# Kernel tuning notes

Measured on AMD Instinct MI355X. Metric: run time of the kernel, lower is better.

## Reference

```python
import jax, jax.numpy as jnp
import numpy as np

E = 8        # n_routed_experts
K = 4        # num_experts_per_tok
T = 1024     # tokens
H = 1024     # hidden_size
I = 1408     # moe_intermediate_size


def setup_inputs() -> dict:
    key = jax.random.key(0)
    ks = jax.random.split(key, 6)
    hidden_states = jax.random.normal(ks[0], (T, H), jnp.float32)
    rw = jax.random.uniform(ks[1], (T, K), jnp.float32)
    router_weights = rw / jnp.sum(rw, axis=-1, keepdims=True)  # normalized top-k router weights
    selected_experts = jax.random.randint(ks[2], (T, K), 0, E, jnp.int32)
    gate_w = jax.random.normal(ks[3], (E, H, I), jnp.float32) * (H ** -0.5)  # lecun_normal-ish
    up_w = jax.random.normal(ks[4], (E, H, I), jnp.float32) * (H ** -0.5)
    down_w = jax.random.normal(ks[5], (E, I, H), jnp.float32) * (I ** -0.5)
    return {
        'hidden_states': hidden_states,
        'router_weights': router_weights,
        'gate_w': gate_w,
        'up_w': up_w,
        'down_w': down_w,
        'selected_experts': selected_experts,
    }


def _grouped_matmul(x, w, seg):
    # x: [m, k] tokens sorted by expert; w: [E, k, n]; seg: [m] expert id per row.
    # Grouped GEMM expressed as E masked GEMMs (fixed small loop over experts);
    # a custom kernel would do true variable-group-size grouped GEMM.
    out = jnp.zeros((x.shape[0], w.shape[-1]), x.dtype)
    for e in range(w.shape[0]):
        out = out + jnp.where((seg == e)[:, None], x, jnp.zeros((), x.dtype)) @ w[e]
    return out


def reference(hidden_states, router_weights, gate_w, up_w, down_w, selected_experts):
    t, k = selected_experts.shape
    flat = selected_experts.ravel()                       # [t*k]
    hs = jnp.repeat(hidden_states, k, axis=0)             # [t*k, H]
    sort_idx = jnp.argsort(flat)                          # dispatch: sort tokens by expert
    seg = flat[sort_idx]
    xs = hs[sort_idx]
    gate = _grouped_matmul(xs, gate_w, seg)               # [t*k, I]
    up = _grouped_matmul(xs, up_w, seg)                   # [t*k, I]
    h = jax.nn.silu(gate) * up                            # fused SwiGLU
    down = _grouped_matmul(h, down_w, seg)                # [t*k, H]
    unsort = jnp.argsort(sort_idx)                        # scatter back to token order
    out = down[unsort].reshape(t, k, -1)
    return jnp.sum(out * router_weights[..., None], axis=1)  # weighted combine [t, H]
```

## Files before the change

### kernel.cpp

```cpp
#include <hip/hip_runtime.h>
#include <hip/hip_bf16.h>
#include <cstdint>
#include <cstddef>

#define NE 8
#define NT 1024
#define NK 4
#define NH 1024
#define NI 1408
#define NA (NT * NK)
#define BM 128
#define MAXTILES 40
#define PADSLOTS 5120

typedef short short8 __attribute__((ext_vector_type(8)));
typedef float f32x4 __attribute__((ext_vector_type(4)));
typedef float f4v __attribute__((ext_vector_type(4)));
typedef unsigned short u16;

#define WS_HDR   0
#define WS_SORT  1024
#define WS_XBF   21504
#define WS_GT    2118656
#define WS_UT    25187328
#define WS_DT    48256000
#define WS_HB    71324672
#define WS_SLOT  (WS_HB + 4992 * NI * 2)

__device__ __forceinline__ u16 f2b(float f) {
  union { float f; uint32_t u; } c; c.f = f;
  uint32_t u = c.u;
  return (u16)((u + 0x7FFFu + ((u >> 16) & 1u)) >> 16);
}

__device__ __forceinline__ void llds16(const void* g, void* l) {
  __builtin_amdgcn_global_load_lds(
      (const __attribute__((address_space(1))) void*)g,
      (__attribute__((address_space(3))) void*)l, 16, 0, 0);
}

__device__ __forceinline__ void transcvt_stripe(const float* __restrict__ src,
                                                u16* __restrict__ dst,
                                                int K, int N, int k0, int n0,
                                                u16* smem, int tid) {
  u16 (*t2)[64][64] = (u16(*)[64][64])smem;
  int r = tid >> 4, c = tid & 15;
  f4v v[2][4];
#pragma unroll
  for (int t = 0; t < 2; ++t)
#pragma unroll
    for (int i = 0; i < 4; ++i)
      v[t][i] = __builtin_nontemporal_load(
          (const f4v*)&src[(size_t)(k0 + r + 16 * i) * N + n0 + t * 64 + c * 4]);
#pragma unroll
  for (int t = 0; t < 2; ++t)
#pragma unroll
    for (int i = 0; i < 4; ++i) {
      ushort4 o;
      o.x = f2b(v[t][i].x); o.y = f2b(v[t][i].y); o.z = f2b(v[t][i].z); o.w = f2b(v[t][i].w);
      int row = r + 16 * i;
      int sc = (c * 4) ^ (row & 56);
      *(ushort4*)&t2[t][row][sc] = o;
    }
  __syncthreads();
#pragma unroll
  for (int t = 0; t < 2; ++t)
#pragma unroll
    for (int i = 0; i < 2; ++i) {
      int idx = i * 256 + tid;
      int n = idx >> 3, kc = idx & 7;
      int cs = n ^ (kc * 8);
      u16 o[8];
#pragma unroll
      for (int j = 0; j < 8; ++j) o[j] = t2[t][kc * 8 + j][cs];
      *(short8*)&dst[(size_t)(n0 + t * 64 + n) * K + k0 + kc * 8] = *(const short8*)o;
    }
}

__global__ __launch_bounds__(256) void k1_prep(
    const float* __restrict__ gw, const float* __restrict__ uw, const float* __restrict__ dw,
    const float* __restrict__ hs, const int* __restrict__ sel,
    u16* __restrict__ gT, u16* __restrict__ uT, u16* __restrict__ dT, u16* __restrict__ xbf,
    int* __restrict__ hdr, int* __restrict__ sorted, int* __restrict__ slotOf) {
  int tid = threadIdx.x;
  int y = blockIdx.y;
  if (y == 24) {
    for (int i = blockIdx.x * 256 + tid; i * 4 < NT * NH; i += 176 * 256) {
      f4v v = __builtin_nontemporal_load((const f4v*)&hs[i * 4]);
      ushort4 o;
      o.x = f2b(v.x); o.y = f2b(v.y); o.z = f2b(v.z); o.w = f2b(v.w);
      *(ushort4*)&xbf[i * 4] = o;
    }
    return;
  }
  if (y == 25) {
    if (blockIdx.x != 0) return;
    __shared__ int cnt[NE], fill[NE], poff_s[NE + 1];
    if (tid < NE) { cnt[tid] = 0; fill[tid] = 0; }
    __syncthreads();
    for (int i = tid; i < NA; i += 256) atomicAdd(&cnt[sel[i]], 1);
    __syncthreads();
    if (tid == 0) {
      int off = 0, nt = 0;
      for (int e = 0; e < NE; ++e) {
        poff_s[e] = off;
        int tiles = (cnt[e] + BM - 1) / BM;
        for (int j = 0; j < tiles; ++j) { hdr[32 + nt] = e; hdr[80 + nt] = off + j * BM; ++nt; }
        off += tiles * BM;
      }
      poff_s[NE] = off;
      hdr[17] = nt;
      for (int e = 0; e < NE; ++e) hdr[e] = cnt[e];
      for (int e = 0; e <= NE; ++e) hdr[8 + e] = poff_s[e];
    }
    __syncthreads();
    for (int i = tid; i < PADSLOTS; i += 256) sorted[i] = -1;
    __syncthreads();
    for (int i = tid; i < NA; i += 256) {
      int e = sel[i];
      int p = atomicAdd(&fill[e], 1);
      int s = poff_s[e] + p;
      sorted[s] = i;
      slotOf[i] = s;
    }
    return;
  }
  __shared__ u16 smem[2 * 64 * 64];
  if (y < 16) {
    int tensor = y >> 3, e = y & 7;
    const float* src = ((tensor == 0) ? gw : uw) + (size_t)e * NH * NI;
    u16* dst = ((tensor == 0) ? gT : uT) + (size_t)e * NH * NI;
    int nb = blockIdx.x % 11, kb = blockIdx.x / 11;
    transcvt_stripe(src, dst, NH, NI, kb * 64, nb * 128, smem, tid);
  } else {
    int e = y - 16;
    const float* src = dw + (size_t)e * NI * NH;
    u16* dst = dT + (size_t)e * NI * NH;
    int nb = blockIdx.x % 8, kb = blockIdx.x / 8;
    transcvt_stripe(src, dst, NI, NH, kb * 64, nb * 128, smem, tid);
  }
}

__global__ __launch_bounds__(256, 2) void k2_gemm1(
    const u16* __restrict__ xbf, const u16* __restrict__ gT, const u16* __restrict__ uT,
    u16* __restrict__ hbuf, const int* __restrict__ hdr, const int* __restrict__ sorted) {
  __shared__ u16 smem[36864];
  int b = blockIdx.x;
  int tid = threadIdx.x;

  int job = (b & 7) * 55 + (b >> 3);
  int tile = job % 40;
  if (tile >= hdr[17]) return;
  int e = hdr[32 + tile];
  int slot0 = hdr[80 + tile];
  int n0 = (job / 40) * 128;

  const u16* aptr[2];
  const u16 *bgp[2], *bup[2];
#pragma unroll
  for (int s = 0; s < 2; ++s) {
    int idx = s * 256 + tid;
    int row = idx >> 2, c = idx & 3;
    int kc = c ^ (row & 3) ^ ((row >> 2) & 3);
    int as = sorted[slot0 + row];
    int trow = (as >= 0) ? (as >> 2) : 0;
    aptr[s] = xbf + (size_t)trow * NH + kc * 8;
    size_t o = ((size_t)e * NI + n0 + row) * NH + kc * 8;
    bgp[s] = gT + o; bup[s] = uT + o;
  }

  int lane = tid & 63, wave = tid >> 6;
  int wm = wave >> 1, wn = wave & 1;
  int l15 = lane & 15, quad = lane >> 4;
  int pos = ((quad ^ (l15 & 3) ^ ((l15 >> 2) & 3)) & 3) * 8;

  f32x4 accg[4][4] = {}; f32x4 accu[4][4] = {};

#define K2_STAGE(BUF, KT)                                                \
  {                                                                      \
    int ko_ = (KT) * 32;                                                 \
    u16* p_ = smem + (BUF) * 12288;                                      \
    llds16(aptr[0] + ko_, p_ + tid * 8);                                 \
    llds16(aptr[1] + ko_, p_ + (256 + tid) * 8);                         \
    llds16(bgp[0] + ko_, p_ + 4096 + tid * 8);                           \
    llds16(bgp[1] + ko_, p_ + 4096 + (256 + tid) * 8);                   \
    llds16(bup[0] + ko_, p_ + 8192 + tid * 8);                           \
    llds16(bup[1] + ko_, p_ + 8192 + (256 + tid) * 8);                   \
  }

  K2_STAGE(0, 0);
  K2_STAGE(1, 1);
  for (int kt = 0; kt < 32; ++kt) {
    if (kt == 31) { asm volatile("s_waitcnt vmcnt(0)" ::: "memory"); }
    else          { asm volatile("s_waitcnt vmcnt(6)" ::: "memory"); }
    __builtin_amdgcn_s_barrier();
    __builtin_amdgcn_sched_barrier(0);
    if (kt < 30) K2_STAGE((kt + 2) % 3, kt + 2);
    const u16* sA  = smem + (kt % 3) * 12288;
    const u16* sBg = sA + 4096;
    const u16* sBu = sA + 8192;
    short8 av[4], bg[4], bu[4];
#pragma unroll
    for (int mf = 0; mf < 4; ++mf)
      av[mf] = *(const short8*)&sA[(wm * 64 + mf * 16 + l15) * 32 + pos];
#pragma unroll
    for (int nf = 0; nf < 4; ++nf) {
      bg[nf] = *(const short8*)&sBg[(wn * 64 + nf * 16 + l15) * 32 + pos];
      bu[nf] = *(const short8*)&sBu[(wn * 64 + nf * 16 + l15) * 32 + pos];
    }
#pragma unroll
    for (int mf = 0; mf < 4; ++mf)
#pragma unroll
      for (int nf = 0; nf < 4; ++nf) {
        accg[mf][nf] = __builtin_amdgcn_mfma_f32_16x16x32_bf16(av[mf], bg[nf], accg[mf][nf], 0, 0, 0);
        accu[mf][nf] = __builtin_amdgcn_mfma_f32_16x16x32_bf16(av[mf], bu[nf], accu[mf][nf], 0, 0, 0);
      }
  }
#undef K2_STAGE

  for (int mf = 0; mf < 4; ++mf)
    for (int nf = 0; nf < 4; ++nf)
      for (int r = 0; r < 4; ++r) {
        int row = wm * 64 + mf * 16 + quad * 4 + r;
        int col = n0 + wn * 64 + nf * 16 + l15;
        float g2 = accg[mf][nf][r], u = accu[mf][nf][r];
        float hv = (g2 / (1.f + __expf(-g2))) * u;
        hbuf[(size_t)(slot0 + row) * NI + col] = f2b(hv);
      }
}

__global__ __launch_bounds__(256, 3) void k3_gemm2(
    const u16* __restrict__ hbuf, const u16* __restrict__ dT,
    const float* __restrict__ rw, float* __restrict__ part,
    const int* __restrict__ hdr, const int* __restrict__ sorted) {
  __shared__ u16 smem[24576];
  int b = blockIdx.x;
  int tile = b >> 3;
  if (tile >= hdr[17]) return;
  int e = hdr[32 + tile];
  int slot0 = hdr[80 + tile];
  int n0 = (b & 7) * 128;
  int tid = threadIdx.x;

  const u16 *ap[2], *bp[2];
#pragma unroll
  for (int s = 0; s < 2; ++s) {
    int idx = s * 256 + tid;
    int row = idx >> 2, c = idx & 3;
    int kc = c ^ (row & 3) ^ ((row >> 2) & 3);
    ap[s] = hbuf + (size_t)(slot0 + row) * NI + kc * 8;
    bp[s] = dT + ((size_t)e * NH + n0 + row) * NI + kc * 8;
  }

  int lane = tid & 63, wave = tid >> 6;
  int wm = wave >> 1, wn = wave & 1;
  int l15 = lane & 15, quad = lane >> 4;
  int pos = ((quad ^ (l15 & 3) ^ ((l15 >> 2) & 3)) & 3) * 8;

  f32x4 acc[4][4] = {};

#define K3_STAGE(BUF, KT)                                                \
  {                                                                      \
    int ko_ = (KT) * 32;                                                 \
    u16* p_ = smem + (BUF) * 8192;                                       \
    llds16(ap[0] + ko_, p_ + tid * 8);                                   \
    llds16(ap[1] + ko_, p_ + (256 + tid) * 8);                           \
    llds16(bp[0] + ko_, p_ + 4096 + tid * 8);                            \
    llds16(bp[1] + ko_, p_ + 4096 + (256 + tid) * 8);                    \
  }

  K3_STAGE(0, 0);
  K3_STAGE(1, 1);
  for (int kt = 0; kt < 44; ++kt) {
    if (kt == 43) { asm volatile("s_waitcnt vmcnt(0)" ::: "memory"); }
    else          { asm volatile("s_waitcnt vmcnt(4)" ::: "memory"); }
    __builtin_amdgcn_s_barrier();
    __builtin_amdgcn_sched_barrier(0);
    if (kt < 42) K3_STAGE((kt + 2) % 3, kt + 2);
    const u16* sA = smem + (kt % 3) * 8192;
    const u16* sB = sA + 4096;
    short8 av[4], bv[4];
#pragma unroll
    for (int mf = 0; mf < 4; ++mf)
      av[mf] = *(const short8*)&sA[(wm * 64 + mf * 16 + l15) * 32 + pos];
#pragma unroll
    for (int nf = 0; nf < 4; ++nf)
      bv[nf] = *(const short8*)&sB[(wn * 64 + nf * 16 + l15) * 32 + pos];
#pragma unroll
    for (int mf = 0; mf < 4; ++mf)
#pragma unroll
      for (int nf = 0; nf < 4; ++nf)
        acc[mf][nf] = __builtin_amdgcn_mfma_f32_16x16x32_bf16(av[mf], bv[nf], acc[mf][nf], 0, 0, 0);
  }
#undef K3_STAGE

  for (int mf = 0; mf < 4; ++mf) {
    int rowb = wm * 64 + mf * 16 + quad * 4;
    for (int r = 0; r < 4; ++r) {
      int slot = slot0 + rowb + r;
      int as = sorted[slot];
      if (as < 0) continue;
      float w = rw[as];
      float* prow = part + (size_t)slot * NH + n0 + wn * 64;
      for (int nf = 0; nf < 4; ++nf)
        prow[nf * 16 + l15] = w * acc[mf][nf][r];
    }
  }
}

__global__ __launch_bounds__(256) void k4_combine(
    const float* __restrict__ part, const int* __restrict__ slotOf,
    float* __restrict__ out) {
  int tid = threadIdx.x;
  int token = blockIdx.x * 2 + (tid >> 7);
  int col0 = (tid & 127) * 8;
  const int* sl = slotOf + token * 4;
  f4v a0 = {0.f, 0.f, 0.f, 0.f}, a1 = {0.f, 0.f, 0.f, 0.f};
#pragma unroll
  for (int k = 0; k < 4; ++k) {
    const float* pr = part + (size_t)sl[k] * NH + col0;
    a0 += *(const f4v*)pr;
    a1 += *(const f4v*)(pr + 4);
  }
  float* o = out + (size_t)token * NH + col0;
  *(f4v*)o = a0;
  *(f4v*)(o + 4) = a1;
}

extern "C" void kernel_launch(void* const* d_in, const int* in_sizes, int n_in,
                              void* d_out, int out_size, void* d_ws, size_t ws_size,
                              hipStream_t stream) {
  const float* hs  = (const float*)d_in[0];
  const float* rw  = (const float*)d_in[1];
  const float* gw  = (const float*)d_in[2];
  const float* uw  = (const float*)d_in[3];
  const float* dw  = (const float*)d_in[4];
  const int*   sel = (const int*)d_in[5];
  float* out = (float*)d_out;

  char* ws = (char*)d_ws;
  int*  hdr    = (int*)(ws + WS_HDR);
  int*  sorted = (int*)(ws + WS_SORT);
  u16*  xbf    = (u16*)(ws + WS_XBF);
  u16*  gT     = (u16*)(ws + WS_GT);
  u16*  uT     = (u16*)(ws + WS_UT);
  u16*  dT     = (u16*)(ws + WS_DT);
  u16*  hb     = (u16*)(ws + WS_HB);
  float* part  = (float*)(ws + WS_GT);
  int*  slotOf = (int*)(ws + WS_SLOT);

  hipLaunchKernelGGL(k1_prep, dim3(176, 26), dim3(256), 0, stream,
                     gw, uw, dw, hs, sel, gT, uT, dT, xbf, hdr, sorted, slotOf);
  hipLaunchKernelGGL(k2_gemm1, dim3(440), dim3(256), 0, stream,
                     xbf, gT, uT, hb, hdr, sorted);
  hipLaunchKernelGGL(k3_gemm2, dim3(320), dim3(256), 0, stream,
                     hb, dT, rw, part, hdr, sorted);
  hipLaunchKernelGGL(k4_combine, dim3(512), dim3(256), 0, stream,
                     part, slotOf, out);
}
```

Baseline: 239.4 us.

## Split down-projection GEMM along K into two partial planes

Splits the second grouped GEMM's reduction dimension into two halves, doubling the grid so more CUs are occupied. Each half writes weighted partials into its own plane of the workspace, and the combine kernel sums both planes. This trades better occupancy and shorter per-block K loops for twice the partial-result write and read traffic.

```diff
diff --git a/kernel.cpp b/kernel.cpp
--- a/kernel.cpp
+++ b/kernel.cpp
@@ -26,6 +26,7 @@
 #define WS_DT    48256000
 #define WS_HB    71324672
 #define WS_SLOT  (WS_HB + 4992 * NI * 2)
+#define PART_PLANE (PADSLOTS * NH)
 
 __device__ __forceinline__ u16 f2b(float f) {
   union { float f; uint32_t u; } c; c.f = f;
@@ -235,11 +236,14 @@
     const int* __restrict__ hdr, const int* __restrict__ sorted) {
   __shared__ u16 smem[24576];
   int b = blockIdx.x;
-  int tile = b >> 3;
+  int nsl = b & 7;
+  int r = b >> 3;
+  int tile = r % 40;
+  int kh = r / 40;
   if (tile >= hdr[17]) return;
   int e = hdr[32 + tile];
   int slot0 = hdr[80 + tile];
-  int n0 = (b & 7) * 128;
+  int n0 = nsl * 128;
   int tid = threadIdx.x;
 
   const u16 *ap[2], *bp[2];
@@ -269,14 +273,15 @@
     llds16(bp[1] + ko_, p_ + 4096 + (256 + tid) * 8);                    \
   }
 
-  K3_STAGE(0, 0);
-  K3_STAGE(1, 1);
-  for (int kt = 0; kt < 44; ++kt) {
-    if (kt == 43) { asm volatile("s_waitcnt vmcnt(0)" ::: "memory"); }
+  int kt0 = kh * 22;
+  K3_STAGE(0, kt0);
+  K3_STAGE(1, kt0 + 1);
+  for (int kt = 0; kt < 22; ++kt) {
+    if (kt == 21) { asm volatile("s_waitcnt vmcnt(0)" ::: "memory"); }
     else          { asm volatile("s_waitcnt vmcnt(4)" ::: "memory"); }
     __builtin_amdgcn_s_barrier();
     __builtin_amdgcn_sched_barrier(0);
-    if (kt < 42) K3_STAGE((kt + 2) % 3, kt + 2);
+    if (kt < 20) K3_STAGE((kt + 2) % 3, kt0 + kt + 2);
     const u16* sA = smem + (kt % 3) * 8192;
     const u16* sB = sA + 4096;
     short8 av[4], bv[4];
@@ -294,16 +299,17 @@
   }
 #undef K3_STAGE
 
+  float* plane = part + (size_t)kh * PART_PLANE;
   for (int mf = 0; mf < 4; ++mf) {
     int rowb = wm * 64 + mf * 16 + quad * 4;
-    for (int r = 0; r < 4; ++r) {
-      int slot = slot0 + rowb + r;
+    for (int rr = 0; rr < 4; ++rr) {
+      int slot = slot0 + rowb + rr;
       int as = sorted[slot];
       if (as < 0) continue;
       float w = rw[as];
-      float* prow = part + (size_t)slot * NH + n0 + wn * 64;
+      float* prow = plane + (size_t)slot * NH + n0 + wn * 64;
       for (int nf = 0; nf < 4; ++nf)
-        prow[nf * 16 + l15] = w * acc[mf][nf][r];
+        prow[nf * 16 + l15] = w * acc[mf][nf][rr];
     }
   }
 }
@@ -318,9 +324,13 @@
   f4v a0 = {0.f, 0.f, 0.f, 0.f}, a1 = {0.f, 0.f, 0.f, 0.f};
 #pragma unroll
   for (int k = 0; k < 4; ++k) {
-    const float* pr = part + (size_t)sl[k] * NH + col0;
-    a0 += *(const f4v*)pr;
-    a1 += *(const f4v*)(pr + 4);
+    size_t ro = (size_t)sl[k] * NH + col0;
+    const float* p0 = part + ro;
+    const float* p1 = part + (size_t)PART_PLANE + ro;
+    a0 += *(const f4v*)p0;
+    a1 += *(const f4v*)(p0 + 4);
+    a0 += *(const f4v*)p1;
+    a1 += *(const f4v*)(p1 + 4);
   }
   float* o = out + (size_t)token * NH + col0;
   *(f4v*)o = a0;
@@ -353,7 +363,7 @@
                      gw, uw, dw, hs, sel, gT, uT, dT, xbf, hdr, sorted, slotOf);
   hipLaunchKernelGGL(k2_gemm1, dim3(440), dim3(256), 0, stream,
                      xbf, gT, uT, hb, hdr, sorted);
-  hipLaunchKernelGGL(k3_gemm2, dim3(320), dim3(256), 0, stream,
+  hipLaunchKernelGGL(k3_gemm2, dim3(640), dim3(256), 0, stream,
                      hb, dT, rw, part, hdr, sorted);
   hipLaunchKernelGGL(k4_combine, dim3(512), dim3(256), 0, stream,
                      part, slotOf, out);
```

Measured after the change: 237.1 us. Within noise of the previous version (-1.0%).
